# Kernel optimization log

Hardware: AMD Instinct MI355X
Metric: run time of the kernel (lower is better)

The kernel has to match this reference:

```python
import jax, jax.numpy as jnp
import numpy as np

N = 4096      # nodes (= maxlen)
E = 4096      # hyperedges
NFEAT = 512
NHID = 512
NHEAD = 8
DK = 64
DV = 64
NLAYER = 4
NCLASS = 16
GAMMA = 0.5
LN_EPS = 1e-5


def _incidence(key):
    # sparse-ish binary incidence matrix with no empty rows/cols
    H = (jax.random.uniform(key, (N, E)) < 0.004).astype(jnp.float32)
    H = H.at[jnp.arange(N), jnp.arange(N) % E].set(1.0)   # every node in >=1 edge
    H = H.at[jnp.arange(E) % N, jnp.arange(E)].set(1.0)   # every edge has >=1 node
    return H


def setup_inputs() -> dict:
    key = jax.random.key(0)
    ks = jax.random.split(key, 16)
    s = 0.02
    inp = {
        "X0": jax.random.normal(ks[0], (N, NFEAT), jnp.float32),
        "H": _incidence(ks[1]),
        "w_feat": jax.random.normal(ks[2], (NFEAT, NHID), jnp.float32) * s,
        "b_feat": jnp.zeros((NHID,), jnp.float32),
        "Wq": jax.random.normal(ks[3], (NLAYER, NHID, NHEAD * DK), jnp.float32) * s,
        "bq": jnp.zeros((NLAYER, NHEAD * DK), jnp.float32),
        "Wk": jax.random.normal(ks[4], (NLAYER, NHID, NHEAD * DK), jnp.float32) * s,
        "bk": jnp.zeros((NLAYER, NHEAD * DK), jnp.float32),
        "Wv": jax.random.normal(ks[5], (NLAYER, NHID, NHEAD * DV), jnp.float32) * s,
        "bv": jnp.zeros((NLAYER, NHEAD * DV), jnp.float32),
        "Wo": jax.random.normal(ks[6], (NLAYER, NHEAD * DV, NHID), jnp.float32) * s,
        "bo": jnp.zeros((NLAYER, NHID), jnp.float32),
        "ln_g": jnp.ones((NLAYER, NHID), jnp.float32),
        "ln_b": jnp.zeros((NLAYER, NHID), jnp.float32),
        "prelu_a": jnp.full((NLAYER,), 0.25, jnp.float32),
        "w_cls": jax.random.normal(ks[7], (NHID, NCLASS), jnp.float32) * s,
        "b_cls": jnp.zeros((NCLASS,), jnp.float32),
    }
    return inp


def _laplace(H):
    # G = DV^-1/2 H W DE^-1 H^T DV^-1/2 with W = I (diag matmuls as broadcasts)
    DV_ = jnp.sum(H, axis=1)                 # [N]
    DE_ = jnp.sum(H, axis=0)                 # [E]
    dv2 = DV_ ** -0.5
    dv2 = dv2.at[0].set(1.0)                 # DV2[0,0] = 1 quirk
    M = (H * (1.0 / DE_)[None, :]) @ H.T     # [N, N]
    return dv2[:, None] * M * dv2[None, :]


def _layer_norm(x, g, b):
    mu = jnp.mean(x, axis=-1, keepdims=True)
    var = jnp.mean((x - mu) ** 2, axis=-1, keepdims=True)
    return (x - mu) * jax.lax.rsqrt(var + LN_EPS) * g + b


def _encoder_layer(x, G, Wq, bq, Wk, bk, Wv, bv, Wo, bo, g, b, a):
    n = x.shape[0]
    q = (x @ Wq + bq).reshape(n, NHEAD, DK)
    k = (x @ Wk + bk).reshape(n, NHEAD, DK)
    v = (x @ Wv + bv).reshape(n, NHEAD, DV)
    scores = jnp.einsum("nhd,mhd->hnm", q, k) / np.sqrt(DK).astype(np.float32)
    attn = jax.nn.softmax(scores, axis=-1)                       # [h, n, n]
    blend = attn * GAMMA + G[None, :, :] * (1.0 - GAMMA)
    ctx = jnp.einsum("hnm,mhd->nhd", blend, v).reshape(n, NHEAD * DV)
    out = _layer_norm(ctx @ Wo + bo + x, g, b)                   # residual = V = x
    out = jnp.where(out >= 0, out, a * out)                      # PReLU (scalar a)
    return out  # dropout is identity at eval


def reference(X0, H, w_feat, b_feat, Wq, bq, Wk, bk, Wv, bv, Wo, bo,
              ln_g, ln_b, prelu_a, w_cls, b_cls):
    G = _laplace(H)
    x = X0 @ w_feat + b_feat
    for i in range(NLAYER):
        x = _encoder_layer(x, G, Wq[i], bq[i], Wk[i], bk[i], Wv[i], bv[i],
                           Wo[i], bo[i], ln_g[i], ln_b[i], prelu_a[i])
    logits = x @ w_cls + b_cls
    return jax.nn.log_softmax(logits, axis=1)
```

## Files before the change

kernel.cpp:

```cpp
#include <hip/hip_runtime.h>
#include <stdint.h>
#include <stddef.h>

typedef unsigned short u16;
typedef __attribute__((ext_vector_type(8))) short short8;
typedef __attribute__((ext_vector_type(4))) float floatx4;

#define NN 4096
#define FD 512
#define NLAYER 4
#define NCLASS 16

__device__ __forceinline__ float b2f(u16 u) {
  union { unsigned int i; float f; } x; x.i = ((unsigned int)u) << 16; return x.f;
}
__device__ __forceinline__ u16 f2b(float f) {
  union { float f; unsigned int i; } x; x.f = f;
  unsigned int r = x.i + 0x7fffu + ((x.i >> 16) & 1u);
  return (u16)(r >> 16);
}
__device__ __forceinline__ int is_f32(const void* Hraw) {
  return ((const u16*)Hraw)[0] == 0;
}
__device__ __forceinline__ float rload(const void* p, size_t i, int f) {
  if (f) { union { unsigned int i; float x; } u; u.i = ((const unsigned int*)p)[i]; return u.x; }
  return b2f(((const u16*)p)[i]);
}
__device__ __forceinline__ void gl2lds16(const void* g, void* l) {
  __builtin_amdgcn_global_load_lds((const __attribute__((address_space(1))) void*)g,
                                   (__attribute__((address_space(3))) void*)l, 16, 0, 0);
}

__global__ __launch_bounds__(256) void gemm_qkv(
    const u16* __restrict__ A, const u16* __restrict__ B, u16* __restrict__ qk,
    u16* __restrict__ vb, u16* __restrict__ vT, int K, long boff,
    const void* __restrict__ bq, const void* __restrict__ bk, const void* __restrict__ bv,
    const void* __restrict__ Hflag)
{
  __shared__ __align__(16) u16 As[64 * 32];
  __shared__ __align__(16) u16 Bs[128 * 32];
  __shared__ u16 Ts[4][16 * 17];
  const int tid = threadIdx.x;
  const int wave = tid >> 6, lane = tid & 63;
  const int wr = (wave >> 1) * 32, wc = (wave & 1) * 64;
  const int srow = lane >> 2;
  const int scol = (((lane & 3) ^ (srow & 3)) * 8);
  const int q4 = lane >> 4, l15 = lane & 15;
  const int sg = l15 & 3;

  floatx4 acc[2][4] = {};
  const u16* Ag = A + (size_t)(blockIdx.y * 64) * K;
  const u16* Bg = B + (size_t)(blockIdx.x * 128) * K;

  for (int k0 = 0; k0 < K; k0 += 32) {
    gl2lds16(Ag + (size_t)(wave * 16 + srow) * K + k0 + scol, &As[wave * 512]);
#pragma unroll
    for (int t = 0; t < 2; t++) {
      const int s = wave * 2 + t;
      gl2lds16(Bg + (size_t)(s * 16 + srow) * K + k0 + scol, &Bs[s * 512]);
    }
    __syncthreads();
    short8 af[2], bf[4];
#pragma unroll
    for (int mt = 0; mt < 2; mt++)
      af[mt] = *(const short8*)&As[(wr + mt * 16 + l15) * 32 + ((q4 ^ sg) * 8)];
#pragma unroll
    for (int nt = 0; nt < 4; nt++)
      bf[nt] = *(const short8*)&Bs[(wc + nt * 16 + l15) * 32 + ((q4 ^ sg) * 8)];
#pragma unroll
    for (int mt = 0; mt < 2; mt++)
#pragma unroll
      for (int nt = 0; nt < 4; nt++)
        acc[mt][nt] = __builtin_amdgcn_mfma_f32_16x16x32_bf16(af[mt], bf[nt], acc[mt][nt], 0, 0, 0);
    __syncthreads();
  }

  const int fl = is_f32(Hflag);
  const int buf = blockIdx.x >> 2;
  const void* bptr = (buf == 0) ? bq : (buf == 1) ? bk : bv;
  const int colbase = (blockIdx.x & 3) * 128;
  const int rowblk = blockIdx.y * 64;

  if (buf < 2) {
    u16* out = qk + (size_t)buf * 2097152;
#pragma unroll
    for (int mt = 0; mt < 2; mt++)
#pragma unroll
      for (int nt = 0; nt < 4; nt++)
#pragma unroll
        for (int r = 0; r < 4; r++) {
          const int row = rowblk + wr + mt * 16 + q4 * 4 + r;
          const int col = colbase + wc + nt * 16 + l15;
          out[(size_t)row * 512 + col] = f2b(acc[mt][nt][r] + rload(bptr, (size_t)boff + col, fl));
        }
  } else {
#pragma unroll
    for (int mt = 0; mt < 2; mt++)
#pragma unroll
      for (int nt = 0; nt < 4; nt++) {
#pragma unroll
        for (int r = 0; r < 4; r++) {
          const int row = rowblk + wr + mt * 16 + q4 * 4 + r;
          const int col = colbase + wc + nt * 16 + l15;
          const u16 val = f2b(acc[mt][nt][r] + rload(bptr, (size_t)boff + col, fl));
          vb[(size_t)row * 512 + col] = val;
          Ts[wave][(q4 * 4 + r) * 17 + l15] = val;
        }
#pragma unroll
        for (int r = 0; r < 4; r++) {
          const u16 tv = Ts[wave][l15 * 17 + q4 * 4 + r];
          const int vrow = colbase + wc + nt * 16 + q4 * 4 + r;
          const int vcol = rowblk + wr + mt * 16 + l15;
          vT[(size_t)vrow * NN + vcol] = tv;
        }
      }
  }
}

template<int EP>
__global__ __launch_bounds__(256) void gemm64_bt(
    const u16* __restrict__ A, const u16* __restrict__ B, u16* __restrict__ C,
    int M, int N, int K,
    const void* __restrict__ bias, long boff,
    const u16* __restrict__ add,
    const void* __restrict__ Hflag)
{
  __shared__ __align__(16) u16 As[64 * 32];
  __shared__ __align__(16) u16 Bs[128 * 32];
  const int tid = threadIdx.x;
  const int wave = tid >> 6, lane = tid & 63;
  const int wr = (wave >> 1) * 32, wc = (wave & 1) * 64;
  const int srow = lane >> 2;
  const int scol = (((lane & 3) ^ (srow & 3)) * 8);
  const int q4 = lane >> 4, l15 = lane & 15;
  const int sg = l15 & 3;

  floatx4 acc[2][4] = {};
  const u16* Ag = A + (size_t)(blockIdx.y * 64) * K;
  const u16* Bg = B + (size_t)(blockIdx.x * 128) * K;

  for (int k0 = 0; k0 < K; k0 += 32) {
    gl2lds16(Ag + (size_t)(wave * 16 + srow) * K + k0 + scol, &As[wave * 512]);
#pragma unroll
    for (int t = 0; t < 2; t++) {
      const int s = wave * 2 + t;
      gl2lds16(Bg + (size_t)(s * 16 + srow) * K + k0 + scol, &Bs[s * 512]);
    }
    __syncthreads();
    short8 af[2], bf[4];
#pragma unroll
    for (int mt = 0; mt < 2; mt++)
      af[mt] = *(const short8*)&As[(wr + mt * 16 + l15) * 32 + ((q4 ^ sg) * 8)];
#pragma unroll
    for (int nt = 0; nt < 4; nt++)
      bf[nt] = *(const short8*)&Bs[(wc + nt * 16 + l15) * 32 + ((q4 ^ sg) * 8)];
#pragma unroll
    for (int mt = 0; mt < 2; mt++)
#pragma unroll
      for (int nt = 0; nt < 4; nt++)
        acc[mt][nt] = __builtin_amdgcn_mfma_f32_16x16x32_bf16(af[mt], bf[nt], acc[mt][nt], 0, 0, 0);
    __syncthreads();
  }

  const int fl = is_f32(Hflag);
#pragma unroll
  for (int mt = 0; mt < 2; mt++)
#pragma unroll
    for (int nt = 0; nt < 4; nt++)
#pragma unroll
      for (int r = 0; r < 4; r++) {
        const int row = blockIdx.y * 64 + wr + mt * 16 + q4 * 4 + r;
        const int col = blockIdx.x * 128 + wc + nt * 16 + l15;
        float v = acc[mt][nt][r];
        if (EP == 2) v += rload(bias, (size_t)boff + col, fl);
        if (EP == 4) v += rload(bias, (size_t)boff + col, fl) + b2f(add[(size_t)row * N + col]);
        C[(size_t)row * N + col] = f2b(v);
      }
}

__global__ __launch_bounds__(256) void flash_attn(
    const u16* __restrict__ q, const u16* __restrict__ k,
    const u16* __restrict__ vT, u16* __restrict__ O0, u16* __restrict__ O1,
    float* __restrict__ lp)
{
  __shared__ __align__(16) u16 Qs[64 * 64];
  __shared__ __align__(16) u16 Ks[2][64 * 64], Vs[2][64 * 64];
  __shared__ __align__(16) u16 Ps[4][16 * 72];
  const int tid = threadIdx.x, wave = tid >> 6, lane = tid & 63;
  const int h = blockIdx.y, q0 = blockIdx.x * 64, z = blockIdx.z;
  const int jbase = z * 2048;
  const int r8 = lane >> 3;
  const int c8 = (((lane & 7) ^ r8) * 8);
  const int q4 = lane >> 4, l15 = lane & 15;
  const int sw = l15 & 7;

#pragma unroll
  for (int t = 0; t < 2; t++) {
    const int s = wave * 2 + t;
    gl2lds16(q + (size_t)(q0 + s * 8 + r8) * FD + h * 64 + c8, &Qs[s * 512]);
    gl2lds16(k + (size_t)(jbase + s * 8 + r8) * FD + h * 64 + c8, &Ks[0][s * 512]);
    gl2lds16(vT + (size_t)(h * 64 + s * 8 + r8) * NN + jbase + c8, &Vs[0][s * 512]);
  }
  __syncthreads();
  const short8 aq0 = *(const short8*)&Qs[(wave * 16 + l15) * 64 + ((q4 ^ sw) * 8)];
  const short8 aq1 = *(const short8*)&Qs[(wave * 16 + l15) * 64 + (((q4 + 4) ^ sw) * 8)];
  short8 vone;
#pragma unroll
  for (int j = 0; j < 8; j++) vone[j] = (short)0x3F80;

  floatx4 O[4] = {};
  floatx4 lacc = {};

  for (int jt = 0; jt < 32; jt++) {
    const int cur = jt & 1;
    if (jt + 1 < 32) {
      const int nb = cur ^ 1;
      const int j0 = jbase + (jt + 1) * 64;
#pragma unroll
      for (int t = 0; t < 2; t++) {
        const int s = wave * 2 + t;
        gl2lds16(k + (size_t)(j0 + s * 8 + r8) * FD + h * 64 + c8, &Ks[nb][s * 512]);
        gl2lds16(vT + (size_t)(h * 64 + s * 8 + r8) * NN + j0 + c8, &Vs[nb][s * 512]);
      }
    }
    floatx4 sacc[4] = {};
#pragma unroll
    for (int nt = 0; nt < 4; nt++) {
      const short8 bk0 = *(const short8*)&Ks[cur][(nt * 16 + l15) * 64 + ((q4 ^ sw) * 8)];
      sacc[nt] = __builtin_amdgcn_mfma_f32_16x16x32_bf16(aq0, bk0, sacc[nt], 0, 0, 0);
      const short8 bk1 = *(const short8*)&Ks[cur][(nt * 16 + l15) * 64 + (((q4 + 4) ^ sw) * 8)];
      sacc[nt] = __builtin_amdgcn_mfma_f32_16x16x32_bf16(aq1, bk1, sacc[nt], 0, 0, 0);
    }
#pragma unroll
    for (int nt = 0; nt < 4; nt++)
#pragma unroll
      for (int r = 0; r < 4; r++) {
        const float pv = __expf(fmaf(sacc[nt][r], 0.125f, -10.f));
        Ps[wave][(q4 * 4 + r) * 72 + nt * 16 + l15] =
            (u16)(__float_as_uint(pv) >> 16);
      }
#pragma unroll
    for (int kk = 0; kk < 2; kk++) {
      const short8 ap = *(const short8*)&Ps[wave][l15 * 72 + kk * 32 + q4 * 8];
#pragma unroll
      for (int dt = 0; dt < 4; dt++) {
        const short8 bv = *(const short8*)&Vs[cur][(dt * 16 + l15) * 64 + (((kk * 4 + q4) ^ sw) * 8)];
        O[dt] = __builtin_amdgcn_mfma_f32_16x16x32_bf16(ap, bv, O[dt], 0, 0, 0);
      }
      lacc = __builtin_amdgcn_mfma_f32_16x16x32_bf16(ap, vone, lacc, 0, 0, 0);
    }
    __syncthreads();
  }
  u16* Op = z ? O1 : O0;
#pragma unroll
  for (int dt = 0; dt < 4; dt++)
#pragma unroll
    for (int r = 0; r < 4; r++)
      Op[(size_t)(q0 + wave * 16 + q4 * 4 + r) * FD + h * 64 + dt * 16 + l15] =
          f2b(O[dt][r]);
  if (l15 == 0)
#pragma unroll
    for (int r = 0; r < 4; r++)
      lp[z * 32768 + h * 4096 + q0 + wave * 16 + q4 * 4 + r] = lacc[r];
}

__global__ __launch_bounds__(256) void spmm_edge(
    const int* __restrict__ offC, const int* __restrict__ nodeList,
    const float* __restrict__ invDE, const float* __restrict__ dv2,
    const u16* __restrict__ vb, float* __restrict__ b)
{
  const int wave = threadIdx.x >> 6, lane = threadIdx.x & 63;
  const int e = blockIdx.x * 4 + wave;
  const int beg = offC[e], end = offC[e + 1];
  float acc[8] = {};
  for (int j = beg; j < end; j++) {
    const int i = nodeList[j];
    const float dvi = dv2[i];
    const short8 row = *(const short8*)&vb[(size_t)i * 512 + lane * 8];
#pragma unroll
    for (int t = 0; t < 8; t++) acc[t] += dvi * b2f((u16)row[t]);
  }
  const float s = invDE[e];
  float4* out = (float4*)&b[(size_t)e * 512 + lane * 8];
  float4 o0, o1;
  o0.x = acc[0] * s; o0.y = acc[1] * s; o0.z = acc[2] * s; o0.w = acc[3] * s;
  o1.x = acc[4] * s; o1.y = acc[5] * s; o1.z = acc[6] * s; o1.w = acc[7] * s;
  out[0] = o0; out[1] = o1;
}

__global__ __launch_bounds__(256) void spmm_node(
    const int* __restrict__ offR, const int* __restrict__ edgeList,
    const float* __restrict__ dv2, const float* __restrict__ b,
    const u16* __restrict__ O0, const u16* __restrict__ O1,
    const float* __restrict__ lp, u16* __restrict__ ctx)
{
  const int wave = threadIdx.x >> 6, lane = threadIdx.x & 63;
  const int i = blockIdx.x * 4 + wave;
  const int beg = offR[i], end = offR[i + 1];
  float acc[8] = {};
  for (int j = beg; j < end; j++) {
    const int e = edgeList[j];
    const float4* bp = (const float4*)&b[(size_t)e * 512 + lane * 8];
    const float4 b0 = bp[0], b1 = bp[1];
    acc[0] += b0.x; acc[1] += b0.y; acc[2] += b0.z; acc[3] += b0.w;
    acc[4] += b1.x; acc[5] += b1.y; acc[6] += b1.z; acc[7] += b1.w;
  }
  const int h = lane >> 3;
  const float invl = 1.f / (lp[h * 4096 + i] + lp[32768 + h * 4096 + i]);
  const float dvi = dv2[i];
  const short8 a0 = *(const short8*)&O0[(size_t)i * 512 + lane * 8];
  const short8 a1 = *(const short8*)&O1[(size_t)i * 512 + lane * 8];
  short8 o;
#pragma unroll
  for (int t = 0; t < 8; t++)
    o[t] = (short)f2b(0.5f * (dvi * acc[t] + (b2f((u16)a0[t]) + b2f((u16)a1[t])) * invl));
  *(short8*)&ctx[(size_t)i * 512 + lane * 8] = o;
}

__global__ __launch_bounds__(256) void degrees_pass1(
    const void* __restrict__ H, float* __restrict__ colpart,
    float* __restrict__ rowsum) {
  __shared__ float cs[NN];
  __shared__ float wsum[16][4];
  const int f = is_f32(H);
  const int tid = threadIdx.x, wave = tid >> 6, lane = tid & 63;
  for (int i = tid; i < NN; i += 256) cs[i] = 0.f;
  __syncthreads();
  const int r0 = blockIdx.x * 16;
  for (int rr = 0; rr < 16; rr++) {
    const size_t rowbase = (size_t)(r0 + rr) * NN;
    float rs = 0.f;
#pragma unroll
    for (int j = 0; j < 16; j++) {
      const int c = tid + j * 256;
      const float v = rload(H, rowbase + c, f);
      cs[c] += v;
      rs += v;
    }
#pragma unroll
    for (int off = 1; off < 64; off <<= 1) rs += __shfl_xor(rs, off);
    if (lane == 0) wsum[rr][wave] = rs;
  }
  __syncthreads();
  if (tid < 16)
    rowsum[r0 + tid] = wsum[tid][0] + wsum[tid][1] + wsum[tid][2] + wsum[tid][3];
  float* cp = colpart + (size_t)blockIdx.x * NN;
  for (int i = tid; i < NN; i += 256) cp[i] = cs[i];
}

__global__ __launch_bounds__(256) void finalize_degrees(
    const float* __restrict__ colpart, float* __restrict__ invDE,
    const float* __restrict__ rowsum, float* __restrict__ dv2,
    float* __restrict__ colsum) {
  __shared__ float red[4][64];
  const int tid = threadIdx.x;
  const int c = tid & 63, pc = tid >> 6;
  const int col = blockIdx.x * 64 + c;
  float s = 0.f;
  for (int p = pc * 64; p < pc * 64 + 64; p++) s += colpart[(size_t)p * NN + col];
  red[pc][c] = s;
  const int r = blockIdx.x * 256 + tid;
  if (r < NN) dv2[r] = (r == 0) ? 1.f : rsqrtf(rowsum[r]);
  __syncthreads();
  if (pc == 0) {
    const float tot = red[0][c] + red[1][c] + red[2][c] + red[3][c];
    colsum[col] = tot;
    invDE[col] = 1.f / tot;
  }
}

__global__ __launch_bounds__(256) void build_offsets(
    const float* __restrict__ rowsum, const float* __restrict__ colsum,
    int* __restrict__ offR, int* __restrict__ offC,
    int* __restrict__ curR, int* __restrict__ curC)
{
  __shared__ int part[256];
  const int tid = threadIdx.x;
  for (int half = 0; half < 2; half++) {
    const float* src = half ? colsum : rowsum;
    int* off = half ? offC : offR;
    int* cur = half ? curC : curR;
    int local[16]; int s = 0;
#pragma unroll
    for (int j = 0; j < 16; j++) { local[j] = s; s += (int)(src[tid * 16 + j] + 0.5f); }
    part[tid] = s;
    __syncthreads();
    for (int d = 1; d < 256; d <<= 1) {
      const int v = (tid >= d) ? part[tid - d] : 0;
      __syncthreads();
      part[tid] += v;
      __syncthreads();
    }
    const int pre = (tid == 0) ? 0 : part[tid - 1];
#pragma unroll
    for (int j = 0; j < 16; j++) {
      const int o = pre + local[j];
      off[tid * 16 + j] = o;
      cur[tid * 16 + j] = o;
    }
    if (tid == 255) off[4096] = part[255];
    __syncthreads();
  }
}

__global__ void fill_csr(const void* __restrict__ H,
                         int* __restrict__ curR, int* __restrict__ curC,
                         int* __restrict__ edgeList, int* __restrict__ nodeList)
{
  const int f = is_f32(H);
  const size_t g = (size_t)blockIdx.x * 256 + threadIdx.x;
  const size_t stride = (size_t)gridDim.x * 256;
  for (size_t idx = g; idx < (size_t)NN * NN; idx += stride) {
    if (rload(H, idx, f) != 0.f) {
      const int i = (int)(idx >> 12);
      const int e = (int)(idx & (NN - 1));
      edgeList[atomicAdd(&curR[i], 1)] = e;
      nodeList[atomicAdd(&curC[e], 1)] = i;
    }
  }
}

__global__ __launch_bounds__(256) void transpose_cvt(
    const void* __restrict__ in, long eoff, u16* __restrict__ out, int R, int C,
    const void* __restrict__ Hflag) {
  __shared__ u16 tile[32][33];
  const int f = is_f32(Hflag);
  const int tx = threadIdx.x & 31, ty = threadIdx.x >> 5;
  const int bx = blockIdx.x, by = blockIdx.y;
#pragma unroll
  for (int kk = 0; kk < 4; kk++)
    tile[ty + kk * 8][tx] =
        f2b(rload(in, (size_t)eoff + (size_t)(by * 32 + ty + kk * 8) * C + bx * 32 + tx, f));
  __syncthreads();
#pragma unroll
  for (int kk = 0; kk < 4; kk++)
    out[(size_t)(bx * 32 + ty + kk * 8) * R + by * 32 + tx] = tile[tx][ty + kk * 8];
}

__global__ __launch_bounds__(256) void transpose_cvt4(
    const void* __restrict__ Wq, const void* __restrict__ Wk,
    const void* __restrict__ Wv, const void* __restrict__ Wo,
    long eoff, u16* __restrict__ wTs, const void* __restrict__ Hflag) {
  __shared__ u16 tile[32][33];
  const int z = blockIdx.z;
  const void* in = (z == 0) ? Wq : (z == 1) ? Wk : (z == 2) ? Wv : Wo;
  u16* out = wTs + (size_t)z * 262144;
  const int f = is_f32(Hflag);
  const int tx = threadIdx.x & 31, ty = threadIdx.x >> 5;
  const int bx = blockIdx.x, by = blockIdx.y;
#pragma unroll
  for (int kk = 0; kk < 4; kk++)
    tile[ty + kk * 8][tx] =
        f2b(rload(in, (size_t)eoff + (size_t)(by * 32 + ty + kk * 8) * 512 + bx * 32 + tx, f));
  __syncthreads();
#pragma unroll
  for (int kk = 0; kk < 4; kk++)
    out[(size_t)(bx * 32 + ty + kk * 8) * 512 + by * 32 + tx] = tile[tx][ty + kk * 8];
}

__global__ void convert_flat(const void* __restrict__ in, u16* __restrict__ out, int n,
                             const void* __restrict__ Hflag) {
  const int f = is_f32(Hflag);
  const int g = blockIdx.x * 256 + threadIdx.x;
  const int stride = gridDim.x * 256;
  for (int i = g; i < n; i += stride) out[i] = f2b(rload(in, i, f));
}

__global__ __launch_bounds__(256) void ln_prelu(
    const u16* __restrict__ pre, const void* __restrict__ g, const void* __restrict__ bb,
    const void* __restrict__ aa, int lidx, u16* __restrict__ X,
    const void* __restrict__ Hflag) {
  const int f = is_f32(Hflag);
  const int tid = threadIdx.x, wave = tid >> 6, lane = tid & 63;
  const int row = blockIdx.x * 4 + wave;
  const short8 raw = *(const short8*)(pre + (size_t)row * FD + lane * 8);
  float v[8], s = 0.f;
#pragma unroll
  for (int j = 0; j < 8; j++) { v[j] = b2f((u16)raw[j]); s += v[j]; }
#pragma unroll
  for (int off = 1; off < 64; off <<= 1) s += __shfl_xor(s, off);
  const float mu = s * (1.f / 512.f);
  float vs = 0.f;
#pragma unroll
  for (int j = 0; j < 8; j++) { const float d = v[j] - mu; vs += d * d; }
#pragma unroll
  for (int off = 1; off < 64; off <<= 1) vs += __shfl_xor(vs, off);
  const float rstd = rsqrtf(vs * (1.f / 512.f) + 1e-5f);
  const float a = rload(aa, lidx, f);
  short8 o;
#pragma unroll
  for (int j = 0; j < 8; j++) {
    float y = (v[j] - mu) * rstd * rload(g, (size_t)lidx * 512 + lane * 8 + j, f)
              + rload(bb, (size_t)lidx * 512 + lane * 8 + j, f);
    y = (y >= 0.f) ? y : a * y;
    o[j] = (short)f2b(y);
  }
  *(short8*)(X + (size_t)row * FD + lane * 8) = o;
}

__global__ __launch_bounds__(256) void cls_logsoftmax(
    const u16* __restrict__ X, const void* __restrict__ w, const void* __restrict__ bc,
    void* __restrict__ out, const void* __restrict__ Hflag) {
  __shared__ float wsm[FD * NCLASS];
  const int f = is_f32(Hflag);
  const int tid = threadIdx.x;
  for (int i = tid; i < FD * NCLASS; i += 256) wsm[i] = rload(w, i, f);
  __syncthreads();
  const int c = tid & 15;
  const int row = blockIdx.x * 16 + (tid >> 4);
  const u16* x = X + (size_t)row * FD;
  float z = rload(bc, c, f);
  for (int kk = 0; kk < FD; kk++) z += b2f(x[kk]) * wsm[kk * NCLASS + c];
  float mx = z;
#pragma unroll
  for (int off = 1; off < 16; off <<= 1) mx = fmaxf(mx, __shfl_xor(mx, off));
  float se = __expf(z - mx);
#pragma unroll
  for (int off = 1; off < 16; off <<= 1) se += __shfl_xor(se, off);
  const float val = z - mx - logf(se);
  if (f) ((float*)out)[(size_t)row * NCLASS + c] = val;
  else   ((u16*)out)[(size_t)row * NCLASS + c] = f2b(val);
}

extern "C" void kernel_launch(void* const* d_in, const int* in_sizes, int n_in,
                              void* d_out, int out_size, void* d_ws, size_t ws_size,
                              hipStream_t stream) {
  const void* X0     = d_in[0];
  const void* H      = d_in[1];
  const void* w_feat = d_in[2];
  const void* b_feat = d_in[3];
  const void* Wq     = d_in[4];
  const void* bq     = d_in[5];
  const void* Wk     = d_in[6];
  const void* bk     = d_in[7];
  const void* Wv     = d_in[8];
  const void* bv     = d_in[9];
  const void* Wo     = d_in[10];
  const void* bo     = d_in[11];
  const void* ln_g   = d_in[12];
  const void* ln_b   = d_in[13];
  const void* pa     = d_in[14];
  const void* w_cls  = d_in[15];
  const void* b_cls  = d_in[16];

  char* ws = (char*)d_ws;
  char* r1 = ws;
  int* offR      = (int*)(r1 + (0 << 10));
  int* offC      = (int*)(r1 + (32 << 10));
  int* curR      = (int*)(r1 + (64 << 10));
  int* curC      = (int*)(r1 + (96 << 10));
  int* edgeList  = (int*)(r1 + ((size_t)1 << 20));
  int* nodeList  = (int*)(r1 + ((size_t)4 << 20));
  float* bbuf    = (float*)(r1 + ((size_t)8 << 20));
  u16* vb        = (u16*)(r1 + ((size_t)16 << 20));
  float* colpart = (float*)(r1 + ((size_t)20 << 20));

  char* r2  = ws + ((size_t)32 << 20);
  u16* qb     = (u16*)(r2 + ((size_t)0  << 20));
  u16* Opart0 = (u16*)(r2 + ((size_t)8  << 20));
  u16* vTb    = (u16*)(r2 + ((size_t)12 << 20));
  u16* ctx    = (u16*)(r2 + ((size_t)16 << 20));
  u16* X      = (u16*)(r2 + ((size_t)20 << 20));
  u16* wTs    = (u16*)(r2 + ((size_t)24 << 20));
  u16* Opart1 = (u16*)(r2 + ((size_t)26 << 20));
  float* lpart = (float*)(r2 + ((size_t)30 << 20));
  u16* opre = qb;
  u16* X0b  = Opart0;

  float* dv2    = (float*)d_out;
  float* invDE  = dv2 + 4096;
  float* rowsum = dv2 + 8192;
  float* colsum = dv2 + 12288;

  degrees_pass1<<<256, 256, 0, stream>>>(H, colpart, rowsum);
  finalize_degrees<<<64, 256, 0, stream>>>(colpart, invDE, rowsum, dv2, colsum);
  build_offsets<<<1, 256, 0, stream>>>(rowsum, colsum, offR, offC, curR, curC);
  fill_csr<<<2048, 256, 0, stream>>>(H, curR, curC, edgeList, nodeList);

  convert_flat<<<2048, 256, 0, stream>>>(X0, X0b, NN * FD, H);
  transpose_cvt<<<dim3(16, 16), 256, 0, stream>>>(w_feat, 0, wTs, 512, 512, H);
  gemm64_bt<2><<<dim3(4, 64), 256, 0, stream>>>(X0b, wTs, X, NN, FD, FD, b_feat, 0, nullptr, H);

  for (int l = 0; l < NLAYER; l++) {
    const long lw = (long)l * 262144;
    transpose_cvt4<<<dim3(16, 16, 4), 256, 0, stream>>>(Wq, Wk, Wv, Wo, lw, wTs, H);

    gemm_qkv<<<dim3(12, 64), 256, 0, stream>>>(X, wTs, qb, vb, vTb, FD, (long)l * 512, bq, bk, bv, H);
    flash_attn<<<dim3(64, 8, 2), 256, 0, stream>>>(qb, qb + 2097152, vTb, Opart0, Opart1, lpart);
    spmm_edge<<<1024, 256, 0, stream>>>(offC, nodeList, invDE, dv2, vb, bbuf);
    spmm_node<<<1024, 256, 0, stream>>>(offR, edgeList, dv2, bbuf, Opart0, Opart1, lpart, ctx);
    gemm64_bt<4><<<dim3(4, 64), 256, 0, stream>>>(ctx, wTs + 3 * 262144, opre, NN, FD, FD, bo, (long)l * 512, X, H);
    ln_prelu<<<1024, 256, 0, stream>>>(opre, ln_g, ln_b, pa, l, X, H);
  }

  cls_logsoftmax<<<256, 256, 0, stream>>>(X, w_cls, b_cls, d_out, H);
}
```

Before: 940.1 us.

## Double query rows per flash-attention block to reuse K/V tiles

Each flash_attn block now handles 128 query rows instead of 64, with each wave computing two 16-row M tiles against the same K/V tiles loaded into shared memory. This halves the K/V global-to-LDS traffic per query and doubles the MFMA work per LDS read of K/V fragments. The cost is a halved grid (512 blocks), more registers for the doubled accumulators, and more LDS per block, any of which may reduce occupancy.

```diff
diff --git a/kernel.cpp b/kernel.cpp
--- a/kernel.cpp
+++ b/kernel.cpp
@@ -183,11 +183,11 @@
     const u16* __restrict__ vT, u16* __restrict__ O0, u16* __restrict__ O1,
     float* __restrict__ lp)
 {
-  __shared__ __align__(16) u16 Qs[64 * 64];
+  __shared__ __align__(16) u16 Qs[128 * 64];
   __shared__ __align__(16) u16 Ks[2][64 * 64], Vs[2][64 * 64];
-  __shared__ __align__(16) u16 Ps[4][16 * 72];
+  __shared__ __align__(16) u16 Ps[4][32 * 72];
   const int tid = threadIdx.x, wave = tid >> 6, lane = tid & 63;
-  const int h = blockIdx.y, q0 = blockIdx.x * 64, z = blockIdx.z;
+  const int h = blockIdx.y, q0 = blockIdx.x * 128, z = blockIdx.z;
   const int jbase = z * 2048;
   const int r8 = lane >> 3;
   const int c8 = (((lane & 7) ^ r8) * 8);
@@ -195,21 +195,29 @@
   const int sw = l15 & 7;
 
 #pragma unroll
+  for (int t = 0; t < 4; t++) {
+    const int s = wave * 4 + t;
+    gl2lds16(q + (size_t)(q0 + s * 8 + r8) * FD + h * 64 + c8, &Qs[s * 512]);
+  }
+#pragma unroll
   for (int t = 0; t < 2; t++) {
     const int s = wave * 2 + t;
-    gl2lds16(q + (size_t)(q0 + s * 8 + r8) * FD + h * 64 + c8, &Qs[s * 512]);
     gl2lds16(k + (size_t)(jbase + s * 8 + r8) * FD + h * 64 + c8, &Ks[0][s * 512]);
     gl2lds16(vT + (size_t)(h * 64 + s * 8 + r8) * NN + jbase + c8, &Vs[0][s * 512]);
   }
   __syncthreads();
-  const short8 aq0 = *(const short8*)&Qs[(wave * 16 + l15) * 64 + ((q4 ^ sw) * 8)];
-  const short8 aq1 = *(const short8*)&Qs[(wave * 16 + l15) * 64 + (((q4 + 4) ^ sw) * 8)];
+  short8 aq[2][2];
+#pragma unroll
+  for (int mt = 0; mt < 2; mt++) {
+    aq[mt][0] = *(const short8*)&Qs[(wave * 32 + mt * 16 + l15) * 64 + ((q4 ^ sw) * 8)];
+    aq[mt][1] = *(const short8*)&Qs[(wave * 32 + mt * 16 + l15) * 64 + (((q4 + 4) ^ sw) * 8)];
+  }
   short8 vone;
 #pragma unroll
   for (int j = 0; j < 8; j++) vone[j] = (short)0x3F80;
 
-  floatx4 O[4] = {};
-  floatx4 lacc = {};
+  floatx4 O[2][4] = {};
+  floatx4 lacc[2] = {};
 
   for (int jt = 0; jt < 32; jt++) {
     const int cur = jt & 1;
@@ -223,45 +231,60 @@
         gl2lds16(vT + (size_t)(h * 64 + s * 8 + r8) * NN + j0 + c8, &Vs[nb][s * 512]);
       }
     }
-    floatx4 sacc[4] = {};
+    floatx4 sacc[2][4] = {};
 #pragma unroll
     for (int nt = 0; nt < 4; nt++) {
       const short8 bk0 = *(const short8*)&Ks[cur][(nt * 16 + l15) * 64 + ((q4 ^ sw) * 8)];
-      sacc[nt] = __builtin_amdgcn_mfma_f32_16x16x32_bf16(aq0, bk0, sacc[nt], 0, 0, 0);
       const short8 bk1 = *(const short8*)&Ks[cur][(nt * 16 + l15) * 64 + (((q4 + 4) ^ sw) * 8)];
-      sacc[nt] = __builtin_amdgcn_mfma_f32_16x16x32_bf16(aq1, bk1, sacc[nt], 0, 0, 0);
-    }
-#pragma unroll
-    for (int nt = 0; nt < 4; nt++)
-#pragma unroll
-      for (int r = 0; r < 4; r++) {
-        const float pv = __expf(fmaf(sacc[nt][r], 0.125f, -10.f));
-        Ps[wave][(q4 * 4 + r) * 72 + nt * 16 + l15] =
-            (u16)(__float_as_uint(pv) >> 16);
+#pragma unroll
+      for (int mt = 0; mt < 2; mt++) {
+        sacc[mt][nt] = __builtin_amdgcn_mfma_f32_16x16x32_bf16(aq[mt][0], bk0, sacc[mt][nt], 0, 0, 0);
+        sacc[mt][nt] = __builtin_amdgcn_mfma_f32_16x16x32_bf16(aq[mt][1], bk1, sacc[mt][nt], 0, 0, 0);
       }
+    }
+#pragma unroll
+    for (int mt = 0; mt < 2; mt++)
+#pragma unroll
+      for (int nt = 0; nt < 4; nt++)
+#pragma unroll
+        for (int r = 0; r < 4; r++) {
+          const float pv = __expf(fmaf(sacc[mt][nt][r], 0.125f, -10.f));
+          Ps[wave][(mt * 16 + q4 * 4 + r) * 72 + nt * 16 + l15] =
+              (u16)(__float_as_uint(pv) >> 16);
+        }
 #pragma unroll
     for (int kk = 0; kk < 2; kk++) {
-      const short8 ap = *(const short8*)&Ps[wave][l15 * 72 + kk * 32 + q4 * 8];
+      short8 ap[2];
+#pragma unroll
+      for (int mt = 0; mt < 2; mt++)
+        ap[mt] = *(const short8*)&Ps[wave][(mt * 16 + l15) * 72 + kk * 32 + q4 * 8];
 #pragma unroll
       for (int dt = 0; dt < 4; dt++) {
         const short8 bv = *(const short8*)&Vs[cur][(dt * 16 + l15) * 64 + (((kk * 4 + q4) ^ sw) * 8)];
-        O[dt] = __builtin_amdgcn_mfma_f32_16x16x32_bf16(ap, bv, O[dt], 0, 0, 0);
+#pragma unroll
+        for (int mt = 0; mt < 2; mt++)
+          O[mt][dt] = __builtin_amdgcn_mfma_f32_16x16x32_bf16(ap[mt], bv, O[mt][dt], 0, 0, 0);
       }
-      lacc = __builtin_amdgcn_mfma_f32_16x16x32_bf16(ap, vone, lacc, 0, 0, 0);
+#pragma unroll
+      for (int mt = 0; mt < 2; mt++)
+        lacc[mt] = __builtin_amdgcn_mfma_f32_16x16x32_bf16(ap[mt], vone, lacc[mt], 0, 0, 0);
     }
     __syncthreads();
   }
   u16* Op = z ? O1 : O0;
 #pragma unroll
-  for (int dt = 0; dt < 4; dt++)
-#pragma unroll
-    for (int r = 0; r < 4; r++)
-      Op[(size_t)(q0 + wave * 16 + q4 * 4 + r) * FD + h * 64 + dt * 16 + l15] =
-          f2b(O[dt][r]);
-  if (l15 == 0)
-#pragma unroll
-    for (int r = 0; r < 4; r++)
-      lp[z * 32768 + h * 4096 + q0 + wave * 16 + q4 * 4 + r] = lacc[r];
+  for (int mt = 0; mt < 2; mt++) {
+#pragma unroll
+    for (int dt = 0; dt < 4; dt++)
+#pragma unroll
+      for (int r = 0; r < 4; r++)
+        Op[(size_t)(q0 + wave * 32 + mt * 16 + q4 * 4 + r) * FD + h * 64 + dt * 16 + l15] =
+            f2b(O[mt][dt][r]);
+    if (l15 == 0)
+#pragma unroll
+      for (int r = 0; r < 4; r++)
+        lp[z * 32768 + h * 4096 + q0 + wave * 32 + mt * 16 + q4 * 4 + r] = lacc[mt][r];
+  }
 }
 
 __global__ __launch_bounds__(256) void spmm_edge(
@@ -586,7 +609,7 @@
     transpose_cvt4<<<dim3(16, 16, 4), 256, 0, stream>>>(Wq, Wk, Wv, Wo, lw, wTs, H);
 
     gemm_qkv<<<dim3(12, 64), 256, 0, stream>>>(X, wTs, qb, vb, vTb, FD, (long)l * 512, bq, bk, bv, H);
-    flash_attn<<<dim3(64, 8, 2), 256, 0, stream>>>(qb, qb + 2097152, vTb, Opart0, Opart1, lpart);
+    flash_attn<<<dim3(32, 8, 2), 256, 0, stream>>>(qb, qb + 2097152, vTb, Opart0, Opart1, lpart);
     spmm_edge<<<1024, 256, 0, stream>>>(offC, nodeList, invDE, dv2, vb, bbuf);
     spmm_node<<<1024, 256, 0, stream>>>(offR, edgeList, dv2, bbuf, Opart0, Opart1, lpart, ctx);
     gemm64_bt<4><<<dim3(4, 64), 256, 0, stream>>>(ctx, wTs + 3 * 262144, opre, NN, FD, FD, bo, (long)l * 512, X, H);
```

Measured after the change: 883.1 us. -6.1%, faster.
